# Performance work log

Measured on AMD Instinct MI355X. Metric: run time of the kernel, lower is better.

## Reference

```python
import jax, jax.numpy as jnp
import numpy as np

EMBED = 768
HEADS = 12
HEAD_DIM = EMBED // HEADS
HIDDEN = 4 * EMBED
EPS = 1e-5


def _layernorm(x, g, b):
    mu = jnp.mean(x, axis=-1, keepdims=True)
    var = jnp.var(x, axis=-1, keepdims=True)
    return (x - mu) * jax.lax.rsqrt(var + EPS) * g + b


def setup_inputs() -> dict:
    key = jax.random.key(0)
    ks = jax.random.split(key, 12)
    s_e = 1.0 / np.sqrt(EMBED)
    s_h = 1.0 / np.sqrt(HIDDEN)
    return {
        "x": jax.random.normal(ks[0], (2, 2048, EMBED), dtype=jnp.float32),
        "ln1_g": jnp.ones((EMBED,), jnp.float32),
        "ln1_b": jnp.zeros((EMBED,), jnp.float32),
        "qkv_w": jax.random.uniform(ks[1], (EMBED, 3 * EMBED), jnp.float32, -s_e, s_e),
        "qkv_b": jax.random.uniform(ks[2], (3 * EMBED,), jnp.float32, -s_e, s_e),
        "proj_w": jax.random.uniform(ks[3], (EMBED, EMBED), jnp.float32, -s_e, s_e),
        "proj_b": jax.random.uniform(ks[4], (EMBED,), jnp.float32, -s_e, s_e),
        "ln2_g": jnp.ones((EMBED,), jnp.float32),
        "ln2_b": jnp.zeros((EMBED,), jnp.float32),
        "fc1_w": jax.random.uniform(ks[5], (EMBED, HIDDEN), jnp.float32, -s_e, s_e),
        "fc1_b": jax.random.uniform(ks[6], (HIDDEN,), jnp.float32, -s_e, s_e),
        "fc2_w": jax.random.uniform(ks[7], (HIDDEN, EMBED), jnp.float32, -s_h, s_h),
        "fc2_b": jax.random.uniform(ks[8], (EMBED,), jnp.float32, -s_h, s_h),
    }


def reference(x, ln1_g, ln1_b, qkv_w, qkv_b, proj_w, proj_b,
              ln2_g, ln2_b, fc1_w, fc1_b, fc2_w, fc2_b):
    B, L, C = x.shape
    scale = HEAD_DIM ** -0.5

    # --- attention sublayer (pre-LN) ---
    h = _layernorm(x, ln1_g, ln1_b)
    qkv = h @ qkv_w + qkv_b                       # [B, L, 3C]
    qkv = qkv.reshape(B, L, 3, HEADS, HEAD_DIM)
    q = jnp.transpose(qkv[:, :, 0], (0, 2, 1, 3))  # [B, H, L, D]
    k = jnp.transpose(qkv[:, :, 1], (0, 2, 1, 3))
    v = jnp.transpose(qkv[:, :, 2], (0, 2, 1, 3))
    attn = jnp.einsum('bhqd,bhkd->bhqk', q, k) * scale  # [B, H, L, L]
    attn = jax.nn.softmax(attn, axis=-1)
    out = jnp.einsum('bhqk,bhkd->bhqd', attn, v)  # [B, H, L, D]
    out = jnp.transpose(out, (0, 2, 1, 3)).reshape(B, L, C)
    x = x + (out @ proj_w + proj_b)

    # --- FFN sublayer (pre-LN) ---
    h = _layernorm(x, ln2_g, ln2_b)
    h = jax.nn.gelu(h @ fc1_w + fc1_b, approximate=False)
    x = x + (h @ fc2_w + fc2_b)
    return x
```

## Files before the change

### kernel.cpp

```cpp
#include <hip/hip_runtime.h>
#include <hip/hip_bf16.h>
#include <math.h>

#define EMBED   768
#define NHEADS  12
#define HD      64
#define HIDDEN  3072
#define SEQ     2048
#define BATCH   2
#define ROWS    (BATCH*SEQ)

#define QSCALE  0.1803368801111204f

typedef __bf16 bf16_t;
typedef __attribute__((ext_vector_type(8))) __bf16 bf16x8;
typedef __attribute__((ext_vector_type(4))) float f32x4;

static __device__ __forceinline__ f32x4 mfma16(bf16x8 a, bf16x8 b, f32x4 c) {
  return __builtin_amdgcn_mfma_f32_16x16x32_bf16(a, b, c, 0, 0, 0);
}

#if __has_builtin(__builtin_amdgcn_exp2f)
static __device__ __forceinline__ float fast_exp2(float x) {
  return __builtin_amdgcn_exp2f(x);
}
#else
static __device__ __forceinline__ float fast_exp2(float x) { return exp2f(x); }
#endif

typedef __attribute__((address_space(1))) const void gas_void;
typedef __attribute__((address_space(3))) void las_void;
static __device__ __forceinline__ void gll16(const void* g, void* l) {
  __builtin_amdgcn_global_load_lds((gas_void*)g, (las_void*)l, 16, 0, 0);
}

__global__ __launch_bounds__(256) void ln_kernel(
    const float* __restrict__ x, const float* __restrict__ g,
    const float* __restrict__ bt, bf16_t* __restrict__ out)
{
  int row = blockIdx.x;
  int tid = threadIdx.x;
  const float* xr = x + (size_t)row * EMBED;
  float v0 = xr[tid], v1 = xr[tid + 256], v2 = xr[tid + 512];
  float s  = v0 + v1 + v2;
  float s2 = v0*v0 + v1*v1 + v2*v2;
  #pragma unroll
  for (int o = 32; o >= 1; o >>= 1) {
    s  += __shfl_xor(s,  o, 64);
    s2 += __shfl_xor(s2, o, 64);
  }
  __shared__ float red[8];
  int wave = tid >> 6, lane = tid & 63;
  if (lane == 0) { red[wave] = s; red[wave + 4] = s2; }
  __syncthreads();
  s  = red[0] + red[1] + red[2] + red[3];
  s2 = red[4] + red[5] + red[6] + red[7];
  float mu  = s * (1.0f / EMBED);
  float var = s2 * (1.0f / EMBED) - mu * mu;
  float rs  = rsqrtf(var + 1e-5f);
  bf16_t* orow = out + (size_t)row * EMBED;
  orow[tid]       = (bf16_t)((v0 - mu) * rs * g[tid]       + bt[tid]);
  orow[tid + 256] = (bf16_t)((v1 - mu) * rs * g[tid + 256] + bt[tid + 256]);
  orow[tid + 512] = (bf16_t)((v2 - mu) * rs * g[tid + 512] + bt[tid + 512]);
}

__global__ __launch_bounds__(256) void transpose_all(
    const float* __restrict__ w0, bf16_t* __restrict__ o0,
    const float* __restrict__ w1, bf16_t* __restrict__ o1,
    const float* __restrict__ w2, bf16_t* __restrict__ o2,
    const float* __restrict__ w3, bf16_t* __restrict__ o3)
{
  __shared__ float tile[32][33];
  int lin = blockIdx.x;
  const float* in; bf16_t* out; int R, C, bx, by;
  if (lin < 1728)      { in = w0; out = o0; R = 768;  C = 2304; lin -= 0;    bx = lin % 72; by = lin / 72; }
  else if (lin < 2304) { in = w1; out = o1; R = 768;  C = 768;  lin -= 1728; bx = lin % 24; by = lin / 24; }
  else if (lin < 4608) { in = w2; out = o2; R = 768;  C = 3072; lin -= 2304; bx = lin % 96; by = lin / 96; }
  else                 { in = w3; out = o3; R = 3072; C = 768;  lin -= 4608; bx = lin % 24; by = lin / 24; }
  int c0 = bx * 32, r0 = by * 32;
  int tx = threadIdx.x & 31, ty = threadIdx.x >> 5;
  #pragma unroll
  for (int p = 0; p < 4; ++p) {
    int r = ty + p * 8;
    tile[r][tx] = in[(size_t)(r0 + r) * C + c0 + tx];
  }
  __syncthreads();
  #pragma unroll
  for (int p = 0; p < 4; ++p) {
    int cc = ty + p * 8;
    out[(size_t)(c0 + cc) * R + r0 + tx] = (bf16_t)tile[tx][cc];
  }
}

__global__ __launch_bounds__(256) void v_transpose(
    const bf16_t* __restrict__ qkv, bf16_t* __restrict__ vt)
{
  __shared__ bf16_t tile[64][68];
  int bh = blockIdx.y;
  int b = bh / NHEADS, h = bh % NHEADS;
  int l0 = blockIdx.x * 64;
  int t = threadIdx.x;
  int dx = (t & 15) * 4;
  int ly = t >> 4;
  #pragma unroll
  for (int p = 0; p < 4; ++p) {
    int l = ly + p * 16;
    const bf16_t* src = qkv + (size_t)(b * SEQ + l0 + l) * 2304 + 1536 + h * HD + dx;
    *(uint2*)&tile[l][dx] = *(const uint2*)src;
  }
  __syncthreads();
  int lx = (t & 15) * 4;
  int dy = t >> 4;
  #pragma unroll
  for (int p = 0; p < 4; ++p) {
    int d = dy + p * 16;
    union { bf16_t h4[4]; uint2 u; } tmp;
    #pragma unroll
    for (int i = 0; i < 4; ++i) tmp.h4[i] = tile[lx + i][d];
    *(uint2*)&vt[((size_t)bh * HD + d) * SEQ + l0 + lx] = tmp.u;
  }
}

template<int MODE, int BN>
__global__ __launch_bounds__(256) void gemm_kernel(
    const bf16_t* __restrict__ A, const bf16_t* __restrict__ WT,
    const float* __restrict__ bias, const float* __restrict__ res,
    void* __restrict__ outp, int N, int K)
{
  constexpr int JT = BN / 32;
  __shared__ bf16_t As[128 * 64];
  __shared__ bf16_t Bs[BN * 64];
  int tid = threadIdx.x;
  int lane = tid & 63, wave = tid >> 6;
  int l15 = lane & 15, quad = lane >> 4;
  int wm = wave >> 1, wn = wave & 1;

  int Nn = N / BN;
  int lin = blockIdx.x;
  int bm = (lin & 7) + 8 * ((lin >> 3) / Nn);
  int bn = (lin >> 3) % Nn;
  int m0 = bm * 128, n0 = bn * BN;

  f32x4 acc[4][JT];
  #pragma unroll
  for (int i = 0; i < 4; ++i)
    #pragma unroll
    for (int j = 0; j < JT; ++j)
      acc[i][j] = (f32x4){0.f, 0.f, 0.f, 0.f};

  int grow = lane >> 3;
  int gcol = ((lane & 7) ^ grow) * 8;
  const bf16_t* abase = A  + (size_t)(m0 + wave * 32 + grow) * K + gcol;
  const bf16_t* bbase = WT + (size_t)(n0 + wave * (BN / 4) + grow) * K + gcol;
  int swk = l15 & 7;

  for (int k0 = 0; k0 < K; k0 += 64) {
    #pragma unroll
    for (int a = 0; a < 4; ++a)
      gll16(abase + (size_t)a * 8 * K + k0, &As[(wave * 32 + a * 8) * 64]);
    #pragma unroll
    for (int a = 0; a < BN / 32; ++a)
      gll16(bbase + (size_t)a * 8 * K + k0, &Bs[(wave * (BN / 4) + a * 8) * 64]);
    __syncthreads();

    #pragma unroll
    for (int g = 0; g < 2; ++g) {
      bf16x8 af[4], bfr[JT];
      #pragma unroll
      for (int i = 0; i < 4; ++i)
        af[i] = *(const bf16x8*)
            &As[(wm * 64 + i * 16 + l15) * 64 + (((g * 4 + quad) ^ swk) * 8)];
      #pragma unroll
      for (int j = 0; j < JT; ++j)
        bfr[j] = *(const bf16x8*)
            &Bs[(wn * (BN / 2) + j * 16 + l15) * 64 + (((g * 4 + quad) ^ swk) * 8)];
      #pragma unroll
      for (int i = 0; i < 4; ++i)
        #pragma unroll
        for (int j = 0; j < JT; ++j)
          acc[i][j] = mfma16(af[i], bfr[j], acc[i][j]);
    }
    __syncthreads();
  }

  #pragma unroll
  for (int i = 0; i < 4; ++i) {
    int mbase = m0 + wm * 64 + i * 16 + quad * 4;
    #pragma unroll
    for (int j = 0; j < JT; ++j) {
      int n = n0 + wn * (BN / 2) + j * 16 + l15;
      float bn_ = bias[n];
      #pragma unroll
      for (int r = 0; r < 4; ++r) {
        size_t idx = (size_t)(mbase + r) * N + n;
        float v = acc[i][j][r] + bn_;
        if (MODE == 1) v = 0.5f * v * (1.0f + erff(v * 0.70710678118654752f));
        if (MODE == 3 && n < 768) v *= QSCALE;
        if (MODE == 2) {
          v += res[idx];
          ((float*)outp)[idx] = v;
        } else {
          ((bf16_t*)outp)[idx] = (bf16_t)v;
        }
      }
    }
  }
}

__global__ __launch_bounds__(256, 2) void attn_kernel(
    const bf16_t* __restrict__ qkv, const bf16_t* __restrict__ vt,
    bf16_t* __restrict__ attnout)
{
  __attribute__((aligned(16))) __shared__ bf16_t smem[4 * 8192 + 4 * 640];
  __shared__ float dsumf[4][128];

  int qt = blockIdx.x, h = blockIdx.y, b = blockIdx.z;
  int tid = threadIdx.x;
  int wave = tid >> 6, lane = tid & 63;
  int l15 = lane & 15, quad = lane >> 4;
  int q0 = qt * 128;
  int bh = b * NHEADS + h;

  bf16_t* wbase = smem + wave * 8192;
  bf16_t* pt    = smem + 32768 + wave * 640;

  bf16x8 bq[8][2];
  #pragma unroll
  for (int qi = 0; qi < 8; ++qi) {
    const bf16_t* qrow = qkv + (size_t)(b * SEQ + q0 + qi * 16 + l15) * 2304
                             + h * HD + quad * 8;
    bq[qi][0] = *(const bf16x8*)qrow;
    bq[qi][1] = *(const bf16x8*)(qrow + 32);
  }
  __asm__ volatile("s_waitcnt vmcnt(0)" ::: "memory");

  f32x4 accO[8][4];
  #pragma unroll
  for (int qi = 0; qi < 8; ++qi)
    #pragma unroll
    for (int t2 = 0; t2 < 4; ++t2)
      accO[qi][t2] = (f32x4){0.f, 0.f, 0.f, 0.f};
  float lpart[8] = {};

  int krow_l = lane >> 3;
  int kchunk = ((lane & 7) ^ krow_l) * 8;
  const bf16_t* ksrc0 = qkv + (size_t)(b * SEQ + wave * 32 + krow_l) * 2304
                            + 768 + h * HD + kchunk;
  int vrow_l = lane >> 2;
  int vchunk = ((lane & 3) ^ (vrow_l & 3)) * 8;
  const bf16_t* vsrc0 = vt + ((size_t)bh * HD + vrow_l) * SEQ + wave * 32 + vchunk;

  constexpr int NIT = SEQ / 128;

  {
    bf16_t* kb = wbase;
    bf16_t* vb = wbase + 2048;
    #pragma unroll
    for (int p = 0; p < 4; ++p) {
      gll16(ksrc0 + (size_t)(p * 8) * 2304, kb + p * 512);
      gll16(vsrc0 + (size_t)(p * 16) * SEQ, vb + p * 512);
    }
  }

  int cb = 0;
  for (int it = 0; it < NIT; ++it) {
    {
      int kvn = ((it + 1) & (NIT - 1)) * 128;
      const bf16_t* ks = ksrc0 + (size_t)kvn * 2304;
      const bf16_t* vs = vsrc0 + kvn;
      bf16_t* kb = wbase + (cb ^ 1) * 4096;
      bf16_t* vb = kb + 2048;
      #pragma unroll
      for (int p = 0; p < 4; ++p) {
        gll16(ks + (size_t)(p * 8) * 2304, kb + p * 512);
        gll16(vs + (size_t)(p * 16) * SEQ, vb + p * 512);
      }
    }
    __asm__ volatile("s_waitcnt vmcnt(8)" ::: "memory");

    const bf16_t* kb = wbase + cb * 4096;
    const bf16_t* vb = kb + 2048;

    bf16x8 ak[2][2];
    #pragma unroll
    for (int t = 0; t < 2; ++t)
      #pragma unroll
      for (int f = 0; f < 2; ++f)
        ak[t][f] = *(const bf16x8*)
            &kb[(t * 16 + l15) * 64 + (((f * 4 + quad) ^ (l15 & 7)) * 8)];

    bf16x8 bv[4];
    #pragma unroll
    for (int t2 = 0; t2 < 4; ++t2)
      bv[t2] = *(const bf16x8*)
          &vb[(t2 * 16 + l15) * 32 + ((quad ^ (l15 & 3)) * 8)];

    #pragma unroll
    for (int qi = 0; qi < 8; ++qi) {
      #pragma unroll
      for (int t = 0; t < 2; ++t) {
        f32x4 s = (f32x4){0.f, 0.f, 0.f, 0.f};
        s = mfma16(ak[t][0], bq[qi][0], s);
        s = mfma16(ak[t][1], bq[qi][1], s);
        union { bf16_t b4[4]; uint2 u; } pk;
        float ls = 0.f;
        #pragma unroll
        for (int r = 0; r < 4; ++r) {
          float pv = fast_exp2(s[r]);
          ls += pv;
          pk.b4[r] = (bf16_t)pv;
        }
        lpart[qi] += ls;
        *(uint2*)&pt[l15 * 40 + t * 16 + quad * 4] = pk.u;
      }
      bf16x8 ap = *(const bf16x8*)&pt[l15 * 40 + quad * 8];
      #pragma unroll
      for (int t2 = 0; t2 < 4; ++t2)
        accO[qi][t2] = mfma16(ap, bv[t2], accO[qi][t2]);
    }
    cb ^= 1;
  }

  #pragma unroll
  for (int qi = 0; qi < 8; ++qi) {
    float l = lpart[qi];
    l += __shfl_xor(l, 16, 64);
    l += __shfl_xor(l, 32, 64);
    if (quad == 0) dsumf[wave][qi * 16 + l15] = l;
  }
  __syncthreads();

  float* slabf = (float*)smem;
  int rq = lane >> 3;
  int d0 = (lane & 7) * 8;

  for (int pass = 0; pass < 4; ++pass) {
    #pragma unroll
    for (int qi2 = 0; qi2 < 2; ++qi2) {
      int qi = pass * 2 + qi2;
      #pragma unroll
      for (int t2 = 0; t2 < 4; ++t2)
        #pragma unroll
        for (int r = 0; r < 4; ++r)
          slabf[wave * 2048 + (qi2 * 16 + quad * 4 + r) * 64 + t2 * 16 + l15]
              = accO[qi][t2][r];
    }
    __syncthreads();
    int q_loc = wave * 8 + rq;
    f32x4 o0 = (f32x4){0.f,0.f,0.f,0.f}, o1 = (f32x4){0.f,0.f,0.f,0.f};
    #pragma unroll
    for (int sw = 0; sw < 4; ++sw) {
      o0 += *(const f32x4*)&slabf[sw * 2048 + q_loc * 64 + d0];
      o1 += *(const f32x4*)&slabf[sw * 2048 + q_loc * 64 + d0 + 4];
    }
    int q_abs = pass * 32 + q_loc;
    float den = dsumf[0][q_abs] + dsumf[1][q_abs] + dsumf[2][q_abs] + dsumf[3][q_abs];
    float inv = 1.0f / den;
    bf16_t ob[8];
    #pragma unroll
    for (int j = 0; j < 4; ++j) {
      ob[j]     = (bf16_t)(o0[j] * inv);
      ob[j + 4] = (bf16_t)(o1[j] * inv);
    }
    *(uint4*)&attnout[(size_t)(b * SEQ + q0 + q_abs) * EMBED + h * HD + d0]
        = *(const uint4*)ob;
    if (pass < 3) __syncthreads();
  }
}

extern "C" void kernel_launch(void* const* d_in, const int* in_sizes, int n_in,
                              void* d_out, int out_size, void* d_ws, size_t ws_size,
                              hipStream_t stream) {
  (void)in_sizes; (void)n_in; (void)out_size; (void)ws_size;
  const float* x      = (const float*)d_in[0];
  const float* ln1_g  = (const float*)d_in[1];
  const float* ln1_b  = (const float*)d_in[2];
  const float* qkv_w  = (const float*)d_in[3];
  const float* qkv_b  = (const float*)d_in[4];
  const float* proj_w = (const float*)d_in[5];
  const float* proj_b = (const float*)d_in[6];
  const float* ln2_g  = (const float*)d_in[7];
  const float* ln2_b  = (const float*)d_in[8];
  const float* fc1_w  = (const float*)d_in[9];
  const float* fc1_b  = (const float*)d_in[10];
  const float* fc2_w  = (const float*)d_in[11];
  const float* fc2_b  = (const float*)d_in[12];
  float* out = (float*)d_out;

  char* p = (char*)d_ws;
  bf16_t* wqkvT  = (bf16_t*)p; p += (size_t)2304 * 768 * 2;
  bf16_t* wprojT = (bf16_t*)p; p += (size_t)768 * 768 * 2;
  bf16_t* wfc1T  = (bf16_t*)p; p += (size_t)3072 * 768 * 2;
  bf16_t* wfc2T  = (bf16_t*)p; p += (size_t)768 * 3072 * 2;
  bf16_t* hbuf   = (bf16_t*)p; p += (size_t)ROWS * 768 * 2;
  bf16_t* qkv    = (bf16_t*)p;
  bf16_t* hid    = (bf16_t*)p; p += (size_t)ROWS * 3072 * 2;
  bf16_t* vt     = (bf16_t*)p; p += (size_t)BATCH * NHEADS * HD * SEQ * 2;
  bf16_t* attno  = (bf16_t*)p; p += (size_t)ROWS * 768 * 2;

  transpose_all<<<6912, 256, 0, stream>>>(qkv_w, wqkvT, proj_w, wprojT,
                                          fc1_w, wfc1T, fc2_w, wfc2T);

  ln_kernel<<<ROWS, 256, 0, stream>>>(x, ln1_g, ln1_b, hbuf);
  gemm_kernel<3,128><<<32 * (2304/128), 256, 0, stream>>>(
      hbuf, wqkvT, qkv_b, nullptr, qkv, 2304, 768);
  v_transpose<<<dim3(SEQ/64, BATCH*NHEADS), 256, 0, stream>>>(qkv, vt);
  attn_kernel<<<dim3(SEQ/128, NHEADS, BATCH), 256, 0, stream>>>(qkv, vt, attno);
  gemm_kernel<2,64><<<32 * (768/64), 256, 0, stream>>>(
      attno, wprojT, proj_b, x, out, 768, 768);

  ln_kernel<<<ROWS, 256, 0, stream>>>(out, ln2_g, ln2_b, hbuf);
  gemm_kernel<1,128><<<32 * (3072/128), 256, 0, stream>>>(
      hbuf, wfc1T, fc1_b, nullptr, hid, 3072, 768);
  gemm_kernel<2,64><<<32 * (768/64), 256, 0, stream>>>(
      hid, wfc2T, fc2_b, out, out, 768, 3072);
}
```

Before: 299.4 us.

## Fuse prep kernels, write V transposed from QKV GEMM, split-K fc2 with atomics

```diff
diff --git a/kernel.cpp b/kernel.cpp
--- a/kernel.cpp
+++ b/kernel.cpp
@@ -32,6 +32,63 @@
 typedef __attribute__((address_space(3))) void las_void;
 static __device__ __forceinline__ void gll16(const void* g, void* l) {
   __builtin_amdgcn_global_load_lds((gas_void*)g, (las_void*)l, 16, 0, 0);
+}
+
+__global__ __launch_bounds__(256) void prep_kernel(
+    const float* __restrict__ w0, bf16_t* __restrict__ o0,
+    const float* __restrict__ w1, bf16_t* __restrict__ o1,
+    const float* __restrict__ w2, bf16_t* __restrict__ o2,
+    const float* __restrict__ w3, bf16_t* __restrict__ o3,
+    const float* __restrict__ x,  const float* __restrict__ g,
+    const float* __restrict__ bt, bf16_t* __restrict__ lnout)
+{
+  __shared__ float tile[32][33];
+  __shared__ float red[8];
+  int lin = blockIdx.x;
+  if (lin < 6912) {
+    const float* in; bf16_t* out; int R, C, bx, by;
+    if (lin < 1728)      { in = w0; out = o0; R = 768;  C = 2304; bx = lin % 72; by = lin / 72; }
+    else if (lin < 2304) { in = w1; out = o1; R = 768;  C = 768;  lin -= 1728; bx = lin % 24; by = lin / 24; }
+    else if (lin < 4608) { in = w2; out = o2; R = 768;  C = 3072; lin -= 2304; bx = lin % 96; by = lin / 96; }
+    else                 { in = w3; out = o3; R = 3072; C = 768;  lin -= 4608; bx = lin % 24; by = lin / 24; }
+    int c0 = bx * 32, r0 = by * 32;
+    int tx = threadIdx.x & 31, ty = threadIdx.x >> 5;
+    #pragma unroll
+    for (int p = 0; p < 4; ++p) {
+      int r = ty + p * 8;
+      tile[r][tx] = in[(size_t)(r0 + r) * C + c0 + tx];
+    }
+    __syncthreads();
+    #pragma unroll
+    for (int p = 0; p < 4; ++p) {
+      int cc = ty + p * 8;
+      out[(size_t)(c0 + cc) * R + r0 + tx] = (bf16_t)tile[tx][cc];
+    }
+    return;
+  }
+  int row = lin - 6912;
+  int tid = threadIdx.x;
+  const float* xr = x + (size_t)row * EMBED;
+  float v0 = xr[tid], v1 = xr[tid + 256], v2 = xr[tid + 512];
+  float s  = v0 + v1 + v2;
+  float s2 = v0*v0 + v1*v1 + v2*v2;
+  #pragma unroll
+  for (int o = 32; o >= 1; o >>= 1) {
+    s  += __shfl_xor(s,  o, 64);
+    s2 += __shfl_xor(s2, o, 64);
+  }
+  int wave = tid >> 6, lane = tid & 63;
+  if (lane == 0) { red[wave] = s; red[wave + 4] = s2; }
+  __syncthreads();
+  s  = red[0] + red[1] + red[2] + red[3];
+  s2 = red[4] + red[5] + red[6] + red[7];
+  float mu  = s * (1.0f / EMBED);
+  float var = s2 * (1.0f / EMBED) - mu * mu;
+  float rs  = rsqrtf(var + 1e-5f);
+  bf16_t* orow = lnout + (size_t)row * EMBED;
+  orow[tid]       = (bf16_t)((v0 - mu) * rs * g[tid]       + bt[tid]);
+  orow[tid + 256] = (bf16_t)((v1 - mu) * rs * g[tid + 256] + bt[tid + 256]);
+  orow[tid + 512] = (bf16_t)((v2 - mu) * rs * g[tid + 512] + bt[tid + 512]);
 }
 
 __global__ __launch_bounds__(256) void ln_kernel(
@@ -64,68 +121,11 @@
   orow[tid + 512] = (bf16_t)((v2 - mu) * rs * g[tid + 512] + bt[tid + 512]);
 }
 
-__global__ __launch_bounds__(256) void transpose_all(
-    const float* __restrict__ w0, bf16_t* __restrict__ o0,
-    const float* __restrict__ w1, bf16_t* __restrict__ o1,
-    const float* __restrict__ w2, bf16_t* __restrict__ o2,
-    const float* __restrict__ w3, bf16_t* __restrict__ o3)
-{
-  __shared__ float tile[32][33];
-  int lin = blockIdx.x;
-  const float* in; bf16_t* out; int R, C, bx, by;
-  if (lin < 1728)      { in = w0; out = o0; R = 768;  C = 2304; lin -= 0;    bx = lin % 72; by = lin / 72; }
-  else if (lin < 2304) { in = w1; out = o1; R = 768;  C = 768;  lin -= 1728; bx = lin % 24; by = lin / 24; }
-  else if (lin < 4608) { in = w2; out = o2; R = 768;  C = 3072; lin -= 2304; bx = lin % 96; by = lin / 96; }
-  else                 { in = w3; out = o3; R = 3072; C = 768;  lin -= 4608; bx = lin % 24; by = lin / 24; }
-  int c0 = bx * 32, r0 = by * 32;
-  int tx = threadIdx.x & 31, ty = threadIdx.x >> 5;
-  #pragma unroll
-  for (int p = 0; p < 4; ++p) {
-    int r = ty + p * 8;
-    tile[r][tx] = in[(size_t)(r0 + r) * C + c0 + tx];
-  }
-  __syncthreads();
-  #pragma unroll
-  for (int p = 0; p < 4; ++p) {
-    int cc = ty + p * 8;
-    out[(size_t)(c0 + cc) * R + r0 + tx] = (bf16_t)tile[tx][cc];
-  }
-}
-
-__global__ __launch_bounds__(256) void v_transpose(
-    const bf16_t* __restrict__ qkv, bf16_t* __restrict__ vt)
-{
-  __shared__ bf16_t tile[64][68];
-  int bh = blockIdx.y;
-  int b = bh / NHEADS, h = bh % NHEADS;
-  int l0 = blockIdx.x * 64;
-  int t = threadIdx.x;
-  int dx = (t & 15) * 4;
-  int ly = t >> 4;
-  #pragma unroll
-  for (int p = 0; p < 4; ++p) {
-    int l = ly + p * 16;
-    const bf16_t* src = qkv + (size_t)(b * SEQ + l0 + l) * 2304 + 1536 + h * HD + dx;
-    *(uint2*)&tile[l][dx] = *(const uint2*)src;
-  }
-  __syncthreads();
-  int lx = (t & 15) * 4;
-  int dy = t >> 4;
-  #pragma unroll
-  for (int p = 0; p < 4; ++p) {
-    int d = dy + p * 16;
-    union { bf16_t h4[4]; uint2 u; } tmp;
-    #pragma unroll
-    for (int i = 0; i < 4; ++i) tmp.h4[i] = tile[lx + i][d];
-    *(uint2*)&vt[((size_t)bh * HD + d) * SEQ + l0 + lx] = tmp.u;
-  }
-}
-
 template<int MODE, int BN>
 __global__ __launch_bounds__(256) void gemm_kernel(
     const bf16_t* __restrict__ A, const bf16_t* __restrict__ WT,
     const float* __restrict__ bias, const float* __restrict__ res,
-    void* __restrict__ outp, int N, int K)
+    void* __restrict__ outp, bf16_t* __restrict__ vt, int N, int K)
 {
   constexpr int JT = BN / 32;
   __shared__ bf16_t As[128 * 64];
@@ -137,6 +137,8 @@
 
   int Nn = N / BN;
   int lin = blockIdx.x;
+  int khalf = 0, k_lo = 0, k_hi = K;
+  if (MODE == 4) { khalf = lin & 1; lin >>= 1; k_lo = khalf * (K / 2); k_hi = k_lo + K / 2; }
   int bm = (lin & 7) + 8 * ((lin >> 3) / Nn);
   int bn = (lin >> 3) % Nn;
   int m0 = bm * 128, n0 = bn * BN;
@@ -154,7 +156,7 @@
   const bf16_t* bbase = WT + (size_t)(n0 + wave * (BN / 4) + grow) * K + gcol;
   int swk = l15 & 7;
 
-  for (int k0 = 0; k0 < K; k0 += 64) {
+  for (int k0 = k_lo; k0 < k_hi; k0 += 64) {
     #pragma unroll
     for (int a = 0; a < 4; ++a)
       gll16(abase + (size_t)a * 8 * K + k0, &As[(wave * 32 + a * 8) * 64]);
@@ -189,7 +191,18 @@
     #pragma unroll
     for (int j = 0; j < JT; ++j) {
       int n = n0 + wn * (BN / 2) + j * 16 + l15;
-      float bn_ = bias[n];
+      float bn_ = (MODE == 4 && khalf != 0) ? 0.f : bias[n];
+      if (MODE == 3 && n >= 1536) {
+        int dcol = n - 1536;
+        int hh = dcol >> 6, dd = dcol & 63;
+        int bsel = mbase >> 11, l = mbase & 2047;
+        union { bf16_t b4[4]; uint2 u; } pk;
+        #pragma unroll
+        for (int r = 0; r < 4; ++r)
+          pk.b4[r] = (bf16_t)(acc[i][j][r] + bn_);
+        *(uint2*)&vt[(((size_t)bsel * NHEADS + hh) * HD + dd) * SEQ + l] = pk.u;
+        continue;
+      }
       #pragma unroll
       for (int r = 0; r < 4; ++r) {
         size_t idx = (size_t)(mbase + r) * N + n;
@@ -199,6 +212,8 @@
         if (MODE == 2) {
           v += res[idx];
           ((float*)outp)[idx] = v;
+        } else if (MODE == 4) {
+          atomicAdd((float*)outp + idx, v);
         } else {
           ((bf16_t*)outp)[idx] = (bf16_t)v;
         }
@@ -211,7 +226,7 @@
     const bf16_t* __restrict__ qkv, const bf16_t* __restrict__ vt,
     bf16_t* __restrict__ attnout)
 {
-  __attribute__((aligned(16))) __shared__ bf16_t smem[4 * 8192 + 4 * 640];
+  __attribute__((aligned(16))) __shared__ bf16_t smem[4 * 4096 + 4 * 640];
   __shared__ float dsumf[4][128];
 
   int qt = blockIdx.x, h = blockIdx.y, b = blockIdx.z;
@@ -221,8 +236,8 @@
   int q0 = qt * 128;
   int bh = b * NHEADS + h;
 
-  bf16_t* wbase = smem + wave * 8192;
-  bf16_t* pt    = smem + 32768 + wave * 640;
+  bf16_t* wbase = smem + wave * 4096;
+  bf16_t* pt    = smem + 16384 + wave * 640;
 
   bf16x8 bq[8][2];
   #pragma unroll
@@ -246,40 +261,32 @@
   int kchunk = ((lane & 7) ^ krow_l) * 8;
   const bf16_t* ksrc0 = qkv + (size_t)(b * SEQ + wave * 32 + krow_l) * 2304
                             + 768 + h * HD + kchunk;
-  int vrow_l = lane >> 2;
-  int vchunk = ((lane & 3) ^ (vrow_l & 3)) * 8;
-  const bf16_t* vsrc0 = vt + ((size_t)bh * HD + vrow_l) * SEQ + wave * 32 + vchunk;
+  const bf16_t* vb0 = vt + ((size_t)bh * HD + l15) * SEQ + wave * 32 + quad * 8;
 
   constexpr int NIT = SEQ / 128;
 
-  {
-    bf16_t* kb = wbase;
-    bf16_t* vb = wbase + 2048;
-    #pragma unroll
-    for (int p = 0; p < 4; ++p) {
-      gll16(ksrc0 + (size_t)(p * 8) * 2304, kb + p * 512);
-      gll16(vsrc0 + (size_t)(p * 16) * SEQ, vb + p * 512);
-    }
-  }
+  #pragma unroll
+  for (int p = 0; p < 4; ++p)
+    gll16(ksrc0 + (size_t)(p * 8) * 2304, wbase + p * 512);
 
   int cb = 0;
   for (int it = 0; it < NIT; ++it) {
+    int kv0 = it * 128;
+    bf16x8 bv[4];
+    #pragma unroll
+    for (int t2 = 0; t2 < 4; ++t2)
+      bv[t2] = *(const bf16x8*)(vb0 + (size_t)(t2 * 16) * SEQ + kv0);
     {
       int kvn = ((it + 1) & (NIT - 1)) * 128;
       const bf16_t* ks = ksrc0 + (size_t)kvn * 2304;
-      const bf16_t* vs = vsrc0 + kvn;
-      bf16_t* kb = wbase + (cb ^ 1) * 4096;
-      bf16_t* vb = kb + 2048;
-      #pragma unroll
-      for (int p = 0; p < 4; ++p) {
+      bf16_t* kb = wbase + (cb ^ 1) * 2048;
+      #pragma unroll
+      for (int p = 0; p < 4; ++p)
         gll16(ks + (size_t)(p * 8) * 2304, kb + p * 512);
-        gll16(vs + (size_t)(p * 16) * SEQ, vb + p * 512);
-      }
-    }
-    __asm__ volatile("s_waitcnt vmcnt(8)" ::: "memory");
-
-    const bf16_t* kb = wbase + cb * 4096;
-    const bf16_t* vb = kb + 2048;
+    }
+    __asm__ volatile("s_waitcnt vmcnt(4)" ::: "memory");
+
+    const bf16_t* kb = wbase + cb * 2048;
 
     bf16x8 ak[2][2];
     #pragma unroll
@@ -288,12 +295,6 @@
       for (int f = 0; f < 2; ++f)
         ak[t][f] = *(const bf16x8*)
             &kb[(t * 16 + l15) * 64 + (((f * 4 + quad) ^ (l15 & 7)) * 8)];
-
-    bf16x8 bv[4];
-    #pragma unroll
-    for (int t2 = 0; t2 < 4; ++t2)
-      bv[t2] = *(const bf16x8*)
-          &vb[(t2 * 16 + l15) * 32 + ((quad ^ (l15 & 3)) * 8)];
 
     #pragma unroll
     for (int qi = 0; qi < 8; ++qi) {
@@ -398,20 +399,19 @@
   bf16_t* vt     = (bf16_t*)p; p += (size_t)BATCH * NHEADS * HD * SEQ * 2;
   bf16_t* attno  = (bf16_t*)p; p += (size_t)ROWS * 768 * 2;
 
-  transpose_all<<<6912, 256, 0, stream>>>(qkv_w, wqkvT, proj_w, wprojT,
-                                          fc1_w, wfc1T, fc2_w, wfc2T);
-
-  ln_kernel<<<ROWS, 256, 0, stream>>>(x, ln1_g, ln1_b, hbuf);
+  prep_kernel<<<6912 + ROWS, 256, 0, stream>>>(
+      qkv_w, wqkvT, proj_w, wprojT, fc1_w, wfc1T, fc2_w, wfc2T,
+      x, ln1_g, ln1_b, hbuf);
+
   gemm_kernel<3,128><<<32 * (2304/128), 256, 0, stream>>>(
-      hbuf, wqkvT, qkv_b, nullptr, qkv, 2304, 768);
-  v_transpose<<<dim3(SEQ/64, BATCH*NHEADS), 256, 0, stream>>>(qkv, vt);
+      hbuf, wqkvT, qkv_b, nullptr, qkv, vt, 2304, 768);
   attn_kernel<<<dim3(SEQ/128, NHEADS, BATCH), 256, 0, stream>>>(qkv, vt, attno);
   gemm_kernel<2,64><<<32 * (768/64), 256, 0, stream>>>(
-      attno, wprojT, proj_b, x, out, 768, 768);
+      attno, wprojT, proj_b, x, out, nullptr, 768, 768);
 
   ln_kernel<<<ROWS, 256, 0, stream>>>(out, ln2_g, ln2_b, hbuf);
   gemm_kernel<1,128><<<32 * (3072/128), 256, 0, stream>>>(
-      hbuf, wfc1T, fc1_b, nullptr, hid, 3072, 768);
-  gemm_kernel<2,64><<<32 * (768/64), 256, 0, stream>>>(
-      hid, wfc2T, fc2_b, out, out, 768, 3072);
-}
+      hbuf, wfc1T, fc1_b, nullptr, hid, nullptr, 3072, 768);
+  gemm_kernel<4,64><<<2 * 32 * (768/64), 256, 0, stream>>>(
+      hid, wfc2T, fc2_b, nullptr, out, nullptr, 768, 3072);
+}
```

Result: faster. 289.7 us (-3.2%).
